# Kernel optimization log

Measured on AMD Instinct MI355X. Metric: run time of the kernel, lower is better.

The kernel has to match this reference:

```python
import jax, jax.numpy as jnp
import numpy as np
from jax.scipy.special import erfc

# ---- static config (matches init_kwargs) ----
N_ATOMS = 16384
NUM_BATCH = 32
N_PAIRS = 1_048_576
KMAX = 8
CUTOFF = 10.0
ON_CUT = 0.25 * CUTOFF   # 2.5
OFF_CUT = 0.75 * CUTOFF  # 7.5
ALPHA = 4.0 / CUTOFF + 0.001
ALPHA2 = ALPHA * ALPHA
TWO_PI = 2.0 * np.pi
ONE_OVER_SQRTPI = 1.0 / np.sqrt(np.pi)
EPS = 1e-8


def _make_kmul():
    r = np.arange(-KMAX, KMAX + 1)
    kx, ky, kz = np.meshgrid(r, r, r, indexing='ij')
    k = np.stack([kx, ky, kz], axis=-1).reshape(-1, 3).astype(np.float32)
    k2 = np.sum(k * k, axis=-1)
    k = k[(k2 > 0) & (k2 <= KMAX ** 2)]  # exclude k=0, spherical cutoff
    return k  # [K, 3]


def setup_inputs() -> dict:
    key = jax.random.key(0)
    ks = jax.random.split(key, 6)
    Qa = 0.5 * jax.random.normal(ks[0], (N_ATOMS,), dtype=jnp.float32)
    rij = 0.5 + 9.5 * jax.random.uniform(ks[1], (N_PAIRS,), dtype=jnp.float32)
    R = 20.0 * jax.random.uniform(ks[2], (N_ATOMS, 3), dtype=jnp.float32)
    boxlen = 18.0 + 4.0 * jax.random.uniform(ks[3], (NUM_BATCH, 3), dtype=jnp.float32)
    cell = boxlen[:, :, None] * jnp.eye(3, dtype=jnp.float32)[None]  # diagonal boxes [B,3,3]
    idx_i = jnp.sort(jax.random.randint(ks[4], (N_PAIRS,), 0, N_ATOMS)).astype(jnp.int32)
    idx_j = jax.random.randint(ks[5], (N_PAIRS,), 0, N_ATOMS).astype(jnp.int32)
    batch_seg = jnp.repeat(jnp.arange(NUM_BATCH, dtype=jnp.int32), N_ATOMS // NUM_BATCH)
    kmul = jnp.asarray(_make_kmul())
    return {"Qa": Qa, "rij": rij, "R": R, "cell": cell, "kmul": kmul,
            "idx_i": idx_i, "idx_j": idx_j, "batch_seg": batch_seg}


def _switch_component(x):
    x_safe = jnp.where(x <= 0, jnp.ones_like(x), x)
    return jnp.where(x <= 0, jnp.zeros_like(x), jnp.exp(-1.0 / x_safe))


def _switch_function(r):
    # smooth C-inf switch: 1 for r<=ON_CUT, 0 for r>=OFF_CUT
    x = (r - ON_CUT) / (OFF_CUT - ON_CUT)
    fp = _switch_component(x)
    fm = _switch_component(1.0 - x)
    return jnp.where(x <= 0, jnp.ones_like(x),
                     jnp.where(x >= 1, jnp.zeros_like(x), fm / (fp + fm)))


def _real_space(Qa, rij, idx_i, idx_j):
    fac = Qa[idx_i] * Qa[idx_j]                    # gather per pair
    f = _switch_function(rij)
    coulomb = 1.0 / rij
    damped = 1.0 / jnp.sqrt(rij * rij + 1.0)
    pw = fac * (f * damped + (1.0 - f) * coulomb) * erfc(ALPHA * rij)
    return jax.ops.segment_sum(pw, idx_i, num_segments=N_ATOMS)  # [N]


def _reciprocal_space(q, R, cell, kmul, batch_seg):
    box_length = jnp.diagonal(cell, axis1=-2, axis2=-1)            # [B,3]
    k = TWO_PI * kmul[None, :, :] / box_length[:, None, :]         # [B,K,3]
    k2 = jnp.sum(k * k, axis=-1)                                   # [B,K]
    qg = jnp.exp(-0.25 * k2 / ALPHA2) / k2                         # [B,K]
    dot = jnp.sum(k[batch_seg] * R[:, None, :], axis=-1)           # [N,K]
    qcos = q[:, None] * jnp.cos(dot)                               # [N,K]
    qsin = q[:, None] * jnp.sin(dot)
    q_real = jax.ops.segment_sum(qcos, batch_seg, num_segments=NUM_BATCH)  # [B,K]
    q_imag = jax.ops.segment_sum(qsin, batch_seg, num_segments=NUM_BATCH)
    qf = q_real * q_real + q_imag * q_imag
    e_recip_b = TWO_PI / jnp.prod(box_length, axis=1) * jnp.sum(qf * qg, axis=-1)  # [B]
    q2 = q * q
    e_self = ALPHA * ONE_OVER_SQRTPI * q2                          # [N]
    w = q2 + EPS
    wnorm = jax.ops.segment_sum(w, batch_seg, num_segments=NUM_BATCH)
    w = w / wnorm[batch_seg]
    return w * e_recip_b[batch_seg] - e_self                       # [N]


def reference(Qa, rij, R, cell, kmul, idx_i, idx_j, batch_seg):
    e_real = _real_space(Qa, rij, idx_i, idx_j)
    e_recip = _reciprocal_space(Qa, R, cell, kmul, batch_seg)
    return e_real + e_recip  # per-atom electrostatic energy [N]
```

## Files before the change

### kernel.cpp

```cpp
#include <hip/hip_runtime.h>

#define N_ATOMS 16384
#define NUM_BATCH 32
#define N_PAIRS 1048576
#define ATOMS_PER_BATCH 512
#define PAIRS_PER_THREAD 16

#define C_TWO_PI 6.2831853071795864769f
#define C_ALPHA 0.401f
#define C_ALPHA2 0.160801f
#define C_SELF 0.22624002f
#define C_EPS 1e-8f

__device__ __forceinline__ float switch_fn(float r) {
    float x = (r - 2.5f) * 0.2f;
    if (x <= 0.0f) return 1.0f;
    if (x >= 1.0f) return 0.0f;
    float fp = __expf(-1.0f / x);
    float fm = __expf(-1.0f / (1.0f - x));
    return fm / (fp + fm);
}

__global__ __launch_bounds__(256) void real_kernel(
    const float* __restrict__ Qa, const float* __restrict__ rij,
    const int* __restrict__ idx_i, const int* __restrict__ idx_j,
    float* __restrict__ out) {
    int t = blockIdx.x * blockDim.x + threadIdx.x;
    long base = (long)t * PAIRS_PER_THREAD;
    const int4*   ii4 = (const int4*)(idx_i + base);
    const int4*   jj4 = (const int4*)(idx_j + base);
    const float4* rr4 = (const float4*)(rij + base);

    int cur = -1;
    float acc = 0.0f;
#pragma unroll
    for (int g = 0; g < PAIRS_PER_THREAD / 4; ++g) {
        int4 ii = ii4[g];
        int4 jj = jj4[g];
        float4 rr = rr4[g];
        int   is[4] = {ii.x, ii.y, ii.z, ii.w};
        int   js[4] = {jj.x, jj.y, jj.z, jj.w};
        float rs[4] = {rr.x, rr.y, rr.z, rr.w};
#pragma unroll
        for (int u = 0; u < 4; ++u) {
            int i = is[u];
            float r = rs[u];
            float f = switch_fn(r);
            float coul   = __builtin_amdgcn_rcpf(r);
            float damped = __builtin_amdgcn_rsqf(fmaf(r, r, 1.0f));
            float fac = Qa[i] * Qa[js[u]];
            float pw = fac * (f * damped + (1.0f - f) * coul) * erfcf(C_ALPHA * r);
            if (i != cur) {
                if (cur >= 0) atomicAdd(out + cur, acc);
                cur = i;
                acc = 0.0f;
            }
            acc += pw;
        }
    }
    if (cur >= 0) atomicAdd(out + cur, acc);
}

#define ASPLIT 4
#define AT_PER_SPLIT (ATOMS_PER_BATCH / ASPLIT)

__global__ __launch_bounds__(64 * ASPLIT) void recip_kernel(
    const float* __restrict__ Qa, const float* __restrict__ R,
    const float* __restrict__ cell, const float* __restrict__ kmul,
    float* __restrict__ e_recip_b, int K) {
    __shared__ float4 at[ATOMS_PER_BATCH];
    __shared__ float pr[ASPLIT][64];
    __shared__ float pi_[ASPLIT][64];

    int b  = blockIdx.y;
    int tx = threadIdx.x;
    int ty = threadIdx.y;
    int flat = ty * 64 + tx;

    float Lx = cell[b * 9 + 0], Ly = cell[b * 9 + 4], Lz = cell[b * 9 + 8];
    float iLx = 1.0f / Lx, iLy = 1.0f / Ly, iLz = 1.0f / Lz;

    int abase = b * ATOMS_PER_BATCH;
    for (int a = flat; a < ATOMS_PER_BATCH; a += 64 * ASPLIT) {
        int n = abase + a;
        at[a] = make_float4(R[3 * n + 0] * iLx, R[3 * n + 1] * iLy,
                            R[3 * n + 2] * iLz, Qa[n]);
    }
    __syncthreads();

    int K2 = K >> 1;
    int kk = K2 + blockIdx.x * 64 + tx;
    bool valid = kk < K;
    int kki = valid ? kk : K2;
    float mx = kmul[3 * kki + 0];
    float my = kmul[3 * kki + 1];
    float mz = kmul[3 * kki + 2];

    float cr = 0.0f, ci = 0.0f;
    int a0 = ty * AT_PER_SPLIT;
#pragma unroll 4
    for (int a = a0; a < a0 + AT_PER_SPLIT; ++a) {
        float4 v = at[a];
        float dr = mx * v.x + my * v.y + mz * v.z;
        float ang = C_TWO_PI * (dr - rintf(dr));
        float s = __sinf(ang);
        float c = __cosf(ang);
        cr = fmaf(v.w, c, cr);
        ci = fmaf(v.w, s, ci);
    }

    if (ty > 0) { pr[ty][tx] = cr; pi_[ty][tx] = ci; }
    __syncthreads();
    if (ty == 0) {
#pragma unroll
        for (int s = 1; s < ASPLIT; ++s) { cr += pr[s][tx]; ci += pi_[s][tx]; }
        float kx = C_TWO_PI * mx * iLx;
        float ky = C_TWO_PI * my * iLy;
        float kz = C_TWO_PI * mz * iLz;
        float k2 = kx * kx + ky * ky + kz * kz;
        float qg = __expf(-0.25f * k2 / C_ALPHA2) / k2;
        float contrib = valid ? 2.0f * (cr * cr + ci * ci) * qg : 0.0f;
#pragma unroll
        for (int off = 32; off > 0; off >>= 1)
            contrib += __shfl_down(contrib, off);
        if (tx == 0) {
            float scale = C_TWO_PI / (Lx * Ly * Lz);
            atomicAdd(e_recip_b + b, scale * contrib);
        }
    }
}

__global__ __launch_bounds__(64) void wnorm_kernel(
    const float* __restrict__ Qa, float* __restrict__ wnorm) {
    int b = blockIdx.x;
    int tid = threadIdx.x;
    float s = 0.0f;
    for (int a = tid; a < ATOMS_PER_BATCH; a += 64) {
        float q = Qa[b * ATOMS_PER_BATCH + a];
        s = fmaf(q, q, s + C_EPS);
    }
#pragma unroll
    for (int off = 32; off > 0; off >>= 1) s += __shfl_down(s, off);
    if (tid == 0) wnorm[b] = s;
}

__global__ __launch_bounds__(256) void final_kernel(
    const float* __restrict__ Qa, const int* __restrict__ batch_seg,
    const float* __restrict__ e_recip_b, const float* __restrict__ wnorm,
    float* __restrict__ out) {
    int n = blockIdx.x * blockDim.x + threadIdx.x;
    if (n >= N_ATOMS) return;
    int b = batch_seg[n];
    float q = Qa[n];
    float q2 = q * q;
    float w = (q2 + C_EPS) / wnorm[b];
    out[n] = out[n] + w * e_recip_b[b] - C_SELF * q2;
}

extern "C" void kernel_launch(void* const* d_in, const int* in_sizes, int n_in,
                              void* d_out, int out_size, void* d_ws, size_t ws_size,
                              hipStream_t stream) {
    const float* Qa   = (const float*)d_in[0];
    const float* rij  = (const float*)d_in[1];
    const float* R    = (const float*)d_in[2];
    const float* cell = (const float*)d_in[3];
    const float* kmul = (const float*)d_in[4];
    const int* idx_i  = (const int*)d_in[5];
    const int* idx_j  = (const int*)d_in[6];
    const int* bseg   = (const int*)d_in[7];
    float* out = (float*)d_out;

    int K = in_sizes[4] / 3;
    int K2 = K / 2;

    float* ws        = (float*)d_ws;
    float* e_recip_b = ws;
    float* wnorm     = ws + 32;

    hipMemsetAsync(d_out, 0, N_ATOMS * sizeof(float), stream);
    hipMemsetAsync(ws, 0, 64 * sizeof(float), stream);

    real_kernel<<<N_PAIRS / PAIRS_PER_THREAD / 256, 256, 0, stream>>>(
        Qa, rij, idx_i, idx_j, out);

    dim3 rblock(64, ASPLIT);
    dim3 rgrid((K2 + 63) / 64, NUM_BATCH);
    recip_kernel<<<rgrid, rblock, 0, stream>>>(Qa, R, cell, kmul, e_recip_b, K);

    wnorm_kernel<<<NUM_BATCH, 64, 0, stream>>>(Qa, wnorm);

    final_kernel<<<(N_ATOMS + 255) / 256, 256, 0, stream>>>(
        Qa, bseg, e_recip_b, wnorm, out);
}
```

Measured before the change: 108.1 us.

## Fuse real-space pass into final kernel using per-atom CSR ranges via binary search

Drops the atomic-based real-space kernel, the wnorm kernel and both memsets. A single final kernel binary-searches the sorted idx_i to find each atom's pair range and sums it with 4 lanes per atom, writing each output once without atomics. The reciprocal kernel writes per-chunk partials that the final kernel reduces, so no zero-initialised accumulator is needed. The cost is a binary search per lane and only 256 blocks of 64 atoms each, with imbalanced pair counts, which may leave the GPU underused compared with the old flat pair-parallel grid.

```diff
diff --git a/kernel.cpp b/kernel.cpp
--- a/kernel.cpp
+++ b/kernel.cpp
@@ -4,9 +4,8 @@
 #define NUM_BATCH 32
 #define N_PAIRS 1048576
 #define ATOMS_PER_BATCH 512
-#define PAIRS_PER_THREAD 16
 
-#define C_TWO_PI 6.2831853071795864769f
+#define C_TWO_PI 6.28318530717958647692f
 #define C_ALPHA 0.401f
 #define C_ALPHA2 0.160801f
 #define C_SELF 0.22624002f
@@ -21,53 +20,12 @@
     return fm / (fp + fm);
 }
 
-__global__ __launch_bounds__(256) void real_kernel(
-    const float* __restrict__ Qa, const float* __restrict__ rij,
-    const int* __restrict__ idx_i, const int* __restrict__ idx_j,
-    float* __restrict__ out) {
-    int t = blockIdx.x * blockDim.x + threadIdx.x;
-    long base = (long)t * PAIRS_PER_THREAD;
-    const int4*   ii4 = (const int4*)(idx_i + base);
-    const int4*   jj4 = (const int4*)(idx_j + base);
-    const float4* rr4 = (const float4*)(rij + base);
+#define ASPLIT 4
 
-    int cur = -1;
-    float acc = 0.0f;
-#pragma unroll
-    for (int g = 0; g < PAIRS_PER_THREAD / 4; ++g) {
-        int4 ii = ii4[g];
-        int4 jj = jj4[g];
-        float4 rr = rr4[g];
-        int   is[4] = {ii.x, ii.y, ii.z, ii.w};
-        int   js[4] = {jj.x, jj.y, jj.z, jj.w};
-        float rs[4] = {rr.x, rr.y, rr.z, rr.w};
-#pragma unroll
-        for (int u = 0; u < 4; ++u) {
-            int i = is[u];
-            float r = rs[u];
-            float f = switch_fn(r);
-            float coul   = __builtin_amdgcn_rcpf(r);
-            float damped = __builtin_amdgcn_rsqf(fmaf(r, r, 1.0f));
-            float fac = Qa[i] * Qa[js[u]];
-            float pw = fac * (f * damped + (1.0f - f) * coul) * erfcf(C_ALPHA * r);
-            if (i != cur) {
-                if (cur >= 0) atomicAdd(out + cur, acc);
-                cur = i;
-                acc = 0.0f;
-            }
-            acc += pw;
-        }
-    }
-    if (cur >= 0) atomicAdd(out + cur, acc);
-}
-
-#define ASPLIT 4
-#define AT_PER_SPLIT (ATOMS_PER_BATCH / ASPLIT)
-
-__global__ __launch_bounds__(64 * ASPLIT) void recip_kernel(
+__global__ __launch_bounds__(256) void recip_kernel(
     const float* __restrict__ Qa, const float* __restrict__ R,
     const float* __restrict__ cell, const float* __restrict__ kmul,
-    float* __restrict__ e_recip_b, int K) {
+    float* __restrict__ partials, int K, int nchunk) {
     __shared__ float4 at[ATOMS_PER_BATCH];
     __shared__ float pr[ASPLIT][64];
     __shared__ float pi_[ASPLIT][64];
@@ -81,7 +39,7 @@
     float iLx = 1.0f / Lx, iLy = 1.0f / Ly, iLz = 1.0f / Lz;
 
     int abase = b * ATOMS_PER_BATCH;
-    for (int a = flat; a < ATOMS_PER_BATCH; a += 64 * ASPLIT) {
+    for (int a = flat; a < ATOMS_PER_BATCH; a += 256) {
         int n = abase + a;
         at[a] = make_float4(R[3 * n + 0] * iLx, R[3 * n + 1] * iLy,
                             R[3 * n + 2] * iLz, Qa[n]);
@@ -97,16 +55,14 @@
     float mz = kmul[3 * kki + 2];
 
     float cr = 0.0f, ci = 0.0f;
-    int a0 = ty * AT_PER_SPLIT;
+    int a0 = ty * (ATOMS_PER_BATCH / ASPLIT);
 #pragma unroll 4
-    for (int a = a0; a < a0 + AT_PER_SPLIT; ++a) {
+    for (int a = a0; a < a0 + (ATOMS_PER_BATCH / ASPLIT); ++a) {
         float4 v = at[a];
         float dr = mx * v.x + my * v.y + mz * v.z;
         float ang = C_TWO_PI * (dr - rintf(dr));
-        float s = __sinf(ang);
-        float c = __cosf(ang);
-        cr = fmaf(v.w, c, cr);
-        ci = fmaf(v.w, s, ci);
+        cr = fmaf(v.w, __cosf(ang), cr);
+        ci = fmaf(v.w, __sinf(ang), ci);
     }
 
     if (ty > 0) { pr[ty][tx] = cr; pi_[ty][tx] = ci; }
@@ -123,38 +79,75 @@
 #pragma unroll
         for (int off = 32; off > 0; off >>= 1)
             contrib += __shfl_down(contrib, off);
-        if (tx == 0) {
-            float scale = C_TWO_PI / (Lx * Ly * Lz);
-            atomicAdd(e_recip_b + b, scale * contrib);
-        }
+        if (tx == 0)
+            partials[b * nchunk + blockIdx.x] =
+                (C_TWO_PI / (Lx * Ly * Lz)) * contrib;
     }
 }
 
-__global__ __launch_bounds__(64) void wnorm_kernel(
-    const float* __restrict__ Qa, float* __restrict__ wnorm) {
-    int b = blockIdx.x;
+#define LPA 4
+#define SUBS 8
+#define APB (ATOMS_PER_BATCH / SUBS)
+
+__global__ __launch_bounds__(256) void final_kernel(
+    const float* __restrict__ Qa, const float* __restrict__ rij,
+    const int* __restrict__ idx_i, const int* __restrict__ idx_j,
+    const float* __restrict__ partials, int nchunk,
+    float* __restrict__ out) {
+    int b   = blockIdx.x >> 3;
+    int sub = blockIdx.x & 7;
     int tid = threadIdx.x;
-    float s = 0.0f;
-    for (int a = tid; a < ATOMS_PER_BATCH; a += 64) {
-        float q = Qa[b * ATOMS_PER_BATCH + a];
-        s = fmaf(q, q, s + C_EPS);
-    }
+    int abase = b * ATOMS_PER_BATCH;
+
+    float q0 = Qa[abase + tid];
+    float q1 = Qa[abase + 256 + tid];
+    float s = fmaf(q0, q0, C_EPS) + fmaf(q1, q1, C_EPS);
 #pragma unroll
     for (int off = 32; off > 0; off >>= 1) s += __shfl_down(s, off);
-    if (tid == 0) wnorm[b] = s;
-}
+    __shared__ float red[4];
+    __shared__ float bc[2];
+    if ((tid & 63) == 0) red[tid >> 6] = s;
+    __syncthreads();
+    if (tid == 0) {
+        float w = red[0] + red[1] + red[2] + red[3];
+        float er = 0.0f;
+        for (int c = 0; c < nchunk; ++c) er += partials[b * nchunk + c];
+        bc[0] = w; bc[1] = er;
+    }
+    __syncthreads();
+    float wnorm   = bc[0];
+    float e_recip = bc[1];
 
-__global__ __launch_bounds__(256) void final_kernel(
-    const float* __restrict__ Qa, const int* __restrict__ batch_seg,
-    const float* __restrict__ e_recip_b, const float* __restrict__ wnorm,
-    float* __restrict__ out) {
-    int n = blockIdx.x * blockDim.x + threadIdx.x;
-    if (n >= N_ATOMS) return;
-    int b = batch_seg[n];
-    float q = Qa[n];
-    float q2 = q * q;
-    float w = (q2 + C_EPS) / wnorm[b];
-    out[n] = out[n] + w * e_recip_b[b] - C_SELF * q2;
+    int atom = abase + sub * APB + (tid >> 2);
+    int g = tid & 3;
+
+    int lo = 0, hi = N_PAIRS;
+    while (lo < hi) { int mid = (lo + hi) >> 1; if (idx_i[mid] < atom) lo = mid + 1; else hi = mid; }
+    int start = lo;
+    lo = 0; hi = N_PAIRS;
+    int key = atom + 1;
+    while (lo < hi) { int mid = (lo + hi) >> 1; if (idx_i[mid] < key) lo = mid + 1; else hi = mid; }
+    int end = lo;
+
+    float qi = Qa[atom];
+    float acc = 0.0f;
+    for (int p = start + g; p < end; p += LPA) {
+        float r = rij[p];
+        float f = switch_fn(r);
+        float coul   = __builtin_amdgcn_rcpf(r);
+        float damped = __builtin_amdgcn_rsqf(fmaf(r, r, 1.0f));
+        float qj = Qa[idx_j[p]];
+        acc = fmaf(qj, (f * damped + (1.0f - f) * coul) * erfcf(C_ALPHA * r), acc);
+    }
+    acc *= qi;
+    acc += __shfl_xor(acc, 1);
+    acc += __shfl_xor(acc, 2);
+
+    if (g == 0) {
+        float q2 = qi * qi;
+        float w = (q2 + C_EPS) / wnorm;
+        out[atom] = acc + w * e_recip - C_SELF * q2;
+    }
 }
 
 extern "C" void kernel_launch(void* const* d_in, const int* in_sizes, int n_in,
@@ -167,28 +160,18 @@
     const float* kmul = (const float*)d_in[4];
     const int* idx_i  = (const int*)d_in[5];
     const int* idx_j  = (const int*)d_in[6];
-    const int* bseg   = (const int*)d_in[7];
     float* out = (float*)d_out;
 
     int K = in_sizes[4] / 3;
     int K2 = K / 2;
+    int nchunk = (K2 + 63) / 64;
 
-    float* ws        = (float*)d_ws;
-    float* e_recip_b = ws;
-    float* wnorm     = ws + 32;
-
-    hipMemsetAsync(d_out, 0, N_ATOMS * sizeof(float), stream);
-    hipMemsetAsync(ws, 0, 64 * sizeof(float), stream);
-
-    real_kernel<<<N_PAIRS / PAIRS_PER_THREAD / 256, 256, 0, stream>>>(
-        Qa, rij, idx_i, idx_j, out);
+    float* partials = (float*)d_ws;
 
     dim3 rblock(64, ASPLIT);
-    dim3 rgrid((K2 + 63) / 64, NUM_BATCH);
-    recip_kernel<<<rgrid, rblock, 0, stream>>>(Qa, R, cell, kmul, e_recip_b, K);
+    dim3 rgrid(nchunk, NUM_BATCH);
+    recip_kernel<<<rgrid, rblock, 0, stream>>>(Qa, R, cell, kmul, partials, K, nchunk);
 
-    wnorm_kernel<<<NUM_BATCH, 64, 0, stream>>>(Qa, wnorm);
-
-    final_kernel<<<(N_ATOMS + 255) / 256, 256, 0, stream>>>(
-        Qa, bseg, e_recip_b, wnorm, out);
+    final_kernel<<<NUM_BATCH * SUBS, 256, 0, stream>>>(
+        Qa, rij, idx_i, idx_j, partials, nchunk, out);
 }
```

Result: slower. 110.4 us (+2.1%).
